# Performance work log

Hardware: AMD Instinct MI355X
Metric: run time of the kernel (lower is better)

Reference implementation:

```python
import jax, jax.numpy as jnp
import numpy as np

B, T, I, H, C = 64, 2048, 256, 256, 10


def setup_inputs() -> dict:
    key = jax.random.key(0)
    ks = jax.random.split(key, 8)
    s_i = 1.0 / np.sqrt(H)
    return {
        "x": jax.random.normal(ks[0], (B, T, I), dtype=jnp.float32),
        "key_mat": jax.random.normal(ks[1], (I, I), dtype=jnp.float32) * (1.0 / np.sqrt(I)),
        "W_ih": jax.random.uniform(ks[2], (4 * H, I), jnp.float32, -s_i, s_i),
        "W_hh": jax.random.uniform(ks[3], (4 * H, H), jnp.float32, -s_i, s_i),
        "b_ih": jax.random.uniform(ks[4], (4 * H,), jnp.float32, -s_i, s_i),
        "b_hh": jax.random.uniform(ks[5], (4 * H,), jnp.float32, -s_i, s_i),
        "W_cls": jax.random.uniform(ks[6], (C, H), jnp.float32, -s_i, s_i),
        "b_cls": jax.random.uniform(ks[7], (C,), jnp.float32, -s_i, s_i),
    }


def reference(x, key_mat, W_ih, W_hh, b_ih, b_hh, W_cls, b_cls):
    # Keyed LSTM: each timestep input is multiplied by the key matrix before
    # the standard LSTM gate computation. Applying the key per step is
    # mathematically identical to one batched matmul up front.
    xk = jnp.einsum("bti,ij->btj", x, key_mat)              # [B,T,I]
    # Precompute input projections for all timesteps (gate order: i,f,g,o)
    x_proj = jnp.einsum("btj,gj->btg", xk, W_ih) + b_ih      # [B,T,4H]

    def step(carry, xt):
        h, c = carry
        gates = xt + h @ W_hh.T + b_hh                        # [B,4H]
        i_g, f_g, g_g, o_g = jnp.split(gates, 4, axis=-1)
        i_g = jax.nn.sigmoid(i_g)
        f_g = jax.nn.sigmoid(f_g)
        g_g = jnp.tanh(g_g)
        o_g = jax.nn.sigmoid(o_g)
        c = f_g * c + i_g * g_g
        h = o_g * jnp.tanh(c)
        return (h, c), None

    h0 = jnp.zeros((x.shape[0], W_hh.shape[1]), x.dtype)
    (h_last, _), _ = jax.lax.scan(step, (h0, h0), jnp.swapaxes(x_proj, 0, 1))
    return h_last @ W_cls.T + b_cls                           # [B,C]
```

## Files before the change

kernel.cpp:

```cpp
#include <hip/hip_runtime.h>
#include <hip/hip_bf16.h>
#include <stdint.h>

#define BB   64
#define TT   2048
#define II   256
#define HH   256
#define G4   1024
#define NC   10

typedef _Float16 half2v __attribute__((ext_vector_type(2)));
typedef _Float16 half8v __attribute__((ext_vector_type(8)));
typedef float    float4v __attribute__((ext_vector_type(4)));

__device__ __forceinline__ float sigmf(float v) { return 1.f / (1.f + __expf(-v)); }
__device__ __forceinline__ float tanhf2(float v) { float e = __expf(2.f * v); return 1.f - 2.f / (e + 1.f); }

__device__ __forceinline__ void bar_lds() {
  asm volatile("s_waitcnt lgkmcnt(0)\n\ts_barrier" ::: "memory");
}

__global__ __launch_bounds__(1024) void prep_wc(
    const float* __restrict__ key, const float* __restrict__ Wih,
    const float* __restrict__ bih, const float* __restrict__ bhh,
    _Float16* __restrict__ WcT, float* __restrict__ biasc) {
  __shared__ float krow[II];
  const int i = blockIdx.x;
  const int g = threadIdx.x;
  if (g < II) krow[g] = key[(size_t)i * II + g];
  __syncthreads();
  const float4* w4 = (const float4*)(Wih + (size_t)g * II);
  float acc = 0.f;
#pragma unroll 8
  for (int j = 0; j < II / 4; ++j) {
    float4 w = w4[j];
    acc += w.x * krow[4 * j] + w.y * krow[4 * j + 1] + w.z * krow[4 * j + 2] + w.w * krow[4 * j + 3];
  }
  WcT[(size_t)g * II + i] = (_Float16)acc;
  if (i == 0) biasc[g] = bih[g] + bhh[g];
}

__global__ __launch_bounds__(256) void prep_wfrag(
    const float* __restrict__ Whh, uint4* __restrict__ wreg, uint4* __restrict__ wldsG) {
  const int id = blockIdx.x * 256 + threadIdx.x;
  const int lane = id & 63;
  const int m  = (id >> 6) & 7;
  const int w  = (id >> 9) & 7;
  const int kt = (id >> 12) & 7;
  const int row = w * 128 + m * 16 + (lane & 15);
  const int k0  = kt * 32 + (lane >> 4) * 8;
  half8v frag;
#pragma unroll
  for (int jj = 0; jj < 8; ++jj) frag[jj] = (_Float16)Whh[(size_t)row * HH + k0 + jj];
  uint4 u = __builtin_bit_cast(uint4, frag);
  if (kt < 6) wreg[((kt * 8 + w) * 8 + m) * 64 + lane] = u;
  else        wldsG[(((kt - 6) * 8 + w) * 8 + m) * 64 + lane] = u;
}

__global__ __launch_bounds__(256) void gemm_xproj(
    const float* __restrict__ x, const _Float16* __restrict__ WcT,
    const float* __restrict__ biasc, _Float16* __restrict__ xpk) {
  __shared__ __align__(16) _Float16 Asm[128][40];
  __shared__ __align__(16) _Float16 Bsm[128][40];
  const int t = threadIdx.x;
  const int n0 = blockIdx.x * 128;
  const int m0 = blockIdx.y * 128;
  const int r = t >> 1;
  const int hoff = (t & 1) * 16;
  const int lane = t & 63, wave = t >> 6;
  const int quad = lane >> 4, l15 = lane & 15;
  const int mh = (wave & 1) * 64, nh = (wave >> 1) * 64;
  float4v zero = {0.f, 0.f, 0.f, 0.f};
  float4v acc[4][4];
#pragma unroll
  for (int a = 0; a < 4; ++a)
#pragma unroll
    for (int b = 0; b < 4; ++b) acc[a][b] = zero;

  for (int kt = 0; kt < 8; ++kt) {
    const int k0 = kt * 32;
    const float4* xa = (const float4*)(x + (size_t)(m0 + r) * II + k0 + hoff);
    float4 f0 = xa[0], f1 = xa[1], f2 = xa[2], f3 = xa[3];
    half8v lo = {(_Float16)f0.x, (_Float16)f0.y, (_Float16)f0.z, (_Float16)f0.w,
                 (_Float16)f1.x, (_Float16)f1.y, (_Float16)f1.z, (_Float16)f1.w};
    half8v hi = {(_Float16)f2.x, (_Float16)f2.y, (_Float16)f2.z, (_Float16)f2.w,
                 (_Float16)f3.x, (_Float16)f3.y, (_Float16)f3.z, (_Float16)f3.w};
    const half8v* bsrc = (const half8v*)(WcT + (size_t)(n0 + r) * II + k0 + hoff);
    half8v b0 = bsrc[0], b1 = bsrc[1];
    *(half8v*)&Asm[r][hoff]     = lo;
    *(half8v*)&Asm[r][hoff + 8] = hi;
    *(half8v*)&Bsm[r][hoff]     = b0;
    *(half8v*)&Bsm[r][hoff + 8] = b1;
    __syncthreads();
    half8v af[4], bf[4];
#pragma unroll
    for (int mt = 0; mt < 4; ++mt) af[mt] = *(const half8v*)&Asm[mh + mt * 16 + l15][quad * 8];
#pragma unroll
    for (int nt = 0; nt < 4; ++nt) bf[nt] = *(const half8v*)&Bsm[nh + nt * 16 + l15][quad * 8];
#pragma unroll
    for (int mt = 0; mt < 4; ++mt)
#pragma unroll
      for (int nt = 0; nt < 4; ++nt)
        acc[mt][nt] = __builtin_amdgcn_mfma_f32_16x16x32_f16(af[mt], bf[nt], acc[mt][nt], 0, 0, 0);
    __syncthreads();
  }
  _Float16* dst = xpk;
#pragma unroll
  for (int nt = 0; nt < 4; ++nt) {
    const int col = n0 + nh + nt * 16 + l15;
    const float bias = biasc[col];
    const int slot16 = (col & 255) * 4 + (col >> 8);
#pragma unroll
    for (int mt = 0; mt < 4; ++mt) {
      const int mrow = m0 + mh + mt * 16 + quad * 4;
#pragma unroll
      for (int j = 0; j < 4; ++j)
        dst[(size_t)(mrow + j) * 1024 + slot16] = (_Float16)(acc[mt][nt][j] + bias);
    }
  }
}

__global__ __launch_bounds__(512, 2) void lstm_seq(
    const uint32_t* __restrict__ xpk, const uint4* __restrict__ wreg,
    const uint4* __restrict__ wldsG, float* __restrict__ hfin) {
  __shared__ __align__(16) _Float16 wsmh[2 * 8 * 8 * 64 * 8];
  __shared__ __align__(16) _Float16 hsh[256];
  __shared__ __align__(16) float gsh[G4];
  const int t0 = threadIdx.x, b = blockIdx.x;
  const int w = t0 >> 6, lane = t0 & 63, quad = lane >> 4;

  half8v wA[48];
#pragma unroll
  for (int kt = 0; kt < 6; ++kt)
#pragma unroll
    for (int m = 0; m < 8; ++m)
      wA[kt * 8 + m] = __builtin_bit_cast(half8v, wreg[((kt * 8 + w) * 8 + m) * 64 + lane]);
#pragma unroll
  for (int i = 0; i < 16; ++i)
    ((uint4*)wsmh)[i * 512 + t0] = wldsG[i * 512 + t0];
  if (t0 < 128) ((uint32_t*)hsh)[t0] = 0;

  float cst = 0.f, hlast = 0.f;
  const uint2* xq = (const uint2*)xpk + (size_t)b * TT * 256 + t0;
  uint2 xn = {0u, 0u};
  if (t0 < 256) xn = xq[0];
  __syncthreads();

  const float4v zero = {0.f, 0.f, 0.f, 0.f};
  for (int t = 0; t < TT; ++t) {
    const uint2 xw = xn;
    if (t0 < 256) xn = xq[(size_t)((t + 1) & (TT - 1)) * 256];
    float4v acc[8];
#pragma unroll
    for (int kt = 0; kt < 8; ++kt) {
      half8v bf = *(const half8v*)&hsh[kt * 32 + quad * 8];
      if (kt < 6) {
#pragma unroll
        for (int m = 0; m < 8; ++m)
          acc[m] = __builtin_amdgcn_mfma_f32_16x16x32_f16(
              wA[kt * 8 + m], bf, (kt == 0) ? zero : acc[m], 0, 0, 0);
      } else {
#pragma unroll
        for (int m = 0; m < 8; ++m) {
          half8v wf = *(const half8v*)&wsmh[((((kt - 6) * 8 + w) * 8 + m) * 64 + lane) * 8];
          acc[m] = __builtin_amdgcn_mfma_f32_16x16x32_f16(wf, bf, acc[m], 0, 0, 0);
        }
      }
    }
    if ((lane & 15) == 0) {
#pragma unroll
      for (int m = 0; m < 8; ++m)
        *(float4v*)&gsh[w * 128 + m * 16 + quad * 4] = acc[m];
    }
    bar_lds();
    if (t0 < 256) {
      float gi = gsh[t0], gf = gsh[t0 + 256], gg = gsh[t0 + 512], go = gsh[t0 + 768];
      half2v xa = __builtin_bit_cast(half2v, xw.x);
      half2v xb = __builtin_bit_cast(half2v, xw.y);
      float ig = sigmf(gi + (float)xa.x);
      float fg = sigmf(gf + (float)xa.y);
      float g2 = tanhf2(gg + (float)xb.x);
      float og = sigmf(go + (float)xb.y);
      cst = fg * cst + ig * g2;
      hlast = og * tanhf2(cst);
      hsh[t0] = (_Float16)hlast;
    }
    bar_lds();
  }
  if (t0 < 256) hfin[(size_t)b * HH + t0] = hlast;
}

__global__ __launch_bounds__(256) void cls_k(
    const float* __restrict__ hfin, const float* __restrict__ Wcls,
    const float* __restrict__ bcls, float* __restrict__ out) {
  __shared__ float part[4][NC];
  const int b = blockIdx.x, tid = threadIdx.x;
  const int lane = tid & 63, wave = tid >> 6;
  float hv = hfin[(size_t)b * HH + tid];
#pragma unroll
  for (int c = 0; c < NC; ++c) {
    float p = hv * Wcls[c * HH + tid];
#pragma unroll
    for (int off = 32; off >= 1; off >>= 1) p += __shfl_down(p, off, 64);
    if (lane == 0) part[wave][c] = p;
  }
  __syncthreads();
  if (tid < NC) {
    out[(size_t)b * NC + tid] =
        part[0][tid] + part[1][tid] + part[2][tid] + part[3][tid] + bcls[tid];
  }
}

extern "C" void kernel_launch(void* const* d_in, const int* in_sizes, int n_in,
                              void* d_out, int out_size, void* d_ws, size_t ws_size,
                              hipStream_t stream) {
  (void)in_sizes; (void)n_in; (void)out_size; (void)ws_size;
  const float* x    = (const float*)d_in[0];
  const float* key  = (const float*)d_in[1];
  const float* Wih  = (const float*)d_in[2];
  const float* Whh  = (const float*)d_in[3];
  const float* bih  = (const float*)d_in[4];
  const float* bhh  = (const float*)d_in[5];
  const float* Wcls = (const float*)d_in[6];
  const float* bcls = (const float*)d_in[7];
  float* out = (float*)d_out;

  char* ws = (char*)d_ws;
  size_t off = 0;
  uint32_t* xpk  = (uint32_t*)(ws + off); off += (size_t)BB * TT * 512 * 4;
  uint4* wreg    = (uint4*)(ws + off);    off += (size_t)6 * 8 * 8 * 64 * 16;
  uint4* wldsG   = (uint4*)(ws + off);    off += (size_t)2 * 8 * 8 * 64 * 16;
  _Float16* WcT  = (_Float16*)(ws + off); off += (size_t)G4 * II * 2;
  float* biasc   = (float*)(ws + off);    off += (size_t)G4 * 4;
  float* hfin    = (float*)(ws + off);    off += (size_t)BB * HH * 4;

  hipLaunchKernelGGL(prep_wc,   dim3(II),  dim3(G4),  0, stream, key, Wih, bih, bhh, WcT, biasc);
  hipLaunchKernelGGL(prep_wfrag, dim3(128), dim3(256), 0, stream, Whh, wreg, wldsG);
  hipLaunchKernelGGL(gemm_xproj, dim3(G4 / 128, (BB * TT) / 128), dim3(256), 0, stream,
                     x, WcT, biasc, (_Float16*)xpk);
  hipLaunchKernelGGL(lstm_seq, dim3(BB), dim3(512), 0, stream,
                     xpk, wreg, wldsG, hfin);
  hipLaunchKernelGGL(cls_k,    dim3(BB), dim3(256), 0, stream, hfin, Wcls, bcls, out);
}
```

Measured before the change: 4.535 ms.

## Batch 16 sequences per LSTM block using full MFMA N dimension with gate-interleaved rows

The recurrent kernel now processes 16 batch elements per workgroup, using the 16 columns of each MFMA tile for batch instead of a single broadcast hidden vector. W_hh rows are permuted so the four gates of one hidden unit land in one accumulator, which lets the epilogue run directly from registers without the gate shared-memory round trip. The hidden-state fragment layout in LDS changes to match. This cuts the grid from 64 to 4 blocks, so per-step latency grows with 16x the useful MFMA work but far fewer CUs are used, and x-projection loads become strided per lane.

New measurement: 13.76 ms. +203.5%, slower.

```diff
diff --git a/kernel.cpp b/kernel.cpp
--- a/kernel.cpp
+++ b/kernel.cpp
@@ -41,20 +41,26 @@
 }
 
 __global__ __launch_bounds__(256) void prep_wfrag(
-    const float* __restrict__ Whh, uint4* __restrict__ wreg, uint4* __restrict__ wldsG) {
+    const float* __restrict__ Whh, uint4* __restrict__ wrg, uint4* __restrict__ wld) {
   const int id = blockIdx.x * 256 + threadIdx.x;
   const int lane = id & 63;
-  const int m  = (id >> 6) & 7;
-  const int w  = (id >> 9) & 7;
-  const int kt = (id >> 12) & 7;
-  const int row = w * 128 + m * 16 + (lane & 15);
-  const int k0  = kt * 32 + (lane >> 4) * 8;
+  const int mg  = (id >> 6) & 63;
+  const int kt  = id >> 12;
+  const int w = mg >> 3, m = mg & 7;
+  const int rowp = mg * 16 + (lane & 15);
+  const int g = (rowp & 3) * 256 + (rowp >> 2);
+  const int k0 = kt * 32 + (lane >> 4) * 8;
   half8v frag;
 #pragma unroll
-  for (int jj = 0; jj < 8; ++jj) frag[jj] = (_Float16)Whh[(size_t)row * HH + k0 + jj];
+  for (int jj = 0; jj < 8; ++jj) frag[jj] = (_Float16)Whh[(size_t)g * HH + k0 + jj];
   uint4 u = __builtin_bit_cast(uint4, frag);
-  if (kt < 6) wreg[((kt * 8 + w) * 8 + m) * 64 + lane] = u;
-  else        wldsG[(((kt - 6) * 8 + w) * 8 + m) * 64 + lane] = u;
+  const bool tail = (kt >= 6) || (kt == 5 && m >= 6);
+  if (!tail) {
+    wrg[((kt * 8 + m) * 8 + w) * 64 + lane] = u;
+  } else {
+    const int slot = (kt == 5) ? (m - 6) : (2 + (kt - 6) * 8 + m);
+    wld[(slot * 8 + w) * 64 + lane] = u;
+  }
 }
 
 __global__ __launch_bounds__(256) void gemm_xproj(
@@ -121,73 +127,74 @@
 }
 
 __global__ __launch_bounds__(512, 2) void lstm_seq(
-    const uint32_t* __restrict__ xpk, const uint4* __restrict__ wreg,
-    const uint4* __restrict__ wldsG, float* __restrict__ hfin) {
-  __shared__ __align__(16) _Float16 wsmh[2 * 8 * 8 * 64 * 8];
-  __shared__ __align__(16) _Float16 hsh[256];
-  __shared__ __align__(16) float gsh[G4];
-  const int t0 = threadIdx.x, b = blockIdx.x;
-  const int w = t0 >> 6, lane = t0 & 63, quad = lane >> 4;
-
-  half8v wA[48];
+    const uint2* __restrict__ xpk, const uint4* __restrict__ wrg,
+    const uint4* __restrict__ wld, float* __restrict__ hfin) {
+  __shared__ __align__(16) uint4 wsm[18 * 512];
+  __shared__ __align__(16) _Float16 hfr[4096];
+  const int t0 = threadIdx.x;
+  const int w = t0 >> 6, lane = t0 & 63;
+  const int l15 = lane & 15, quad = lane >> 4;
+  const int bb = blockIdx.x * 16;
+
+  half8v wA[46];
 #pragma unroll
   for (int kt = 0; kt < 6; ++kt)
 #pragma unroll
-    for (int m = 0; m < 8; ++m)
-      wA[kt * 8 + m] = __builtin_bit_cast(half8v, wreg[((kt * 8 + w) * 8 + m) * 64 + lane]);
-#pragma unroll
-  for (int i = 0; i < 16; ++i)
-    ((uint4*)wsmh)[i * 512 + t0] = wldsG[i * 512 + t0];
-  if (t0 < 128) ((uint32_t*)hsh)[t0] = 0;
-
-  float cst = 0.f, hlast = 0.f;
-  const uint2* xq = (const uint2*)xpk + (size_t)b * TT * 256 + t0;
-  uint2 xn = {0u, 0u};
-  if (t0 < 256) xn = xq[0];
+    for (int m = 0; m < 8; ++m) {
+      if (kt == 5 && m >= 6) continue;
+      wA[kt * 8 + m] = __builtin_bit_cast(half8v, wrg[((kt * 8 + m) * 8 + w) * 64 + lane]);
+    }
+#pragma unroll
+  for (int i = 0; i < 18; ++i) wsm[i * 512 + t0] = wld[i * 512 + t0];
+#pragma unroll
+  for (int i = 0; i < 4; ++i) ((uint32_t*)hfr)[i * 512 + t0] = 0;
+
+  float c0 = 0.f, c1 = 0.f, c2 = 0.f, c3 = 0.f, c4 = 0.f, c5 = 0.f, c6 = 0.f, c7 = 0.f;
+  const size_t xbase = ((size_t)(bb + l15) * TT) * 256 + (size_t)(w * 32 + quad);
   __syncthreads();
 
   const float4v zero = {0.f, 0.f, 0.f, 0.f};
   for (int t = 0; t < TT; ++t) {
-    const uint2 xw = xn;
-    if (t0 < 256) xn = xq[(size_t)((t + 1) & (TT - 1)) * 256];
+    const size_t xo = xbase + (size_t)t * 256;
+    uint2 x0 = xpk[xo], x1 = xpk[xo + 4], x2 = xpk[xo + 8], x3 = xpk[xo + 12];
+    uint2 x4, x5, x6, x7;
     float4v acc[8];
 #pragma unroll
     for (int kt = 0; kt < 8; ++kt) {
-      half8v bf = *(const half8v*)&hsh[kt * 32 + quad * 8];
-      if (kt < 6) {
-#pragma unroll
-        for (int m = 0; m < 8; ++m)
-          acc[m] = __builtin_amdgcn_mfma_f32_16x16x32_f16(
-              wA[kt * 8 + m], bf, (kt == 0) ? zero : acc[m], 0, 0, 0);
-      } else {
-#pragma unroll
-        for (int m = 0; m < 8; ++m) {
-          half8v wf = *(const half8v*)&wsmh[((((kt - 6) * 8 + w) * 8 + m) * 64 + lane) * 8];
-          acc[m] = __builtin_amdgcn_mfma_f32_16x16x32_f16(wf, bf, acc[m], 0, 0, 0);
+      half8v hb = *(const half8v*)&hfr[kt * 512 + lane * 8];
+      if (kt == 6) { x4 = xpk[xo + 16]; x5 = xpk[xo + 20]; x6 = xpk[xo + 24]; x7 = xpk[xo + 28]; }
+#pragma unroll
+      for (int m = 0; m < 8; ++m) {
+        half8v wf;
+        if (kt < 5 || (kt == 5 && m < 6)) {
+          wf = wA[kt * 8 + m];
+        } else {
+          const int slot = (kt == 5) ? (m - 6) : (2 + (kt - 6) * 8 + m);
+          wf = __builtin_bit_cast(half8v, wsm[slot * 512 + t0]);
         }
+        acc[m] = __builtin_amdgcn_mfma_f32_16x16x32_f16(wf, hb, (kt == 0) ? zero : acc[m], 0, 0, 0);
       }
     }
-    if ((lane & 15) == 0) {
-#pragma unroll
-      for (int m = 0; m < 8; ++m)
-        *(float4v*)&gsh[w * 128 + m * 16 + quad * 4] = acc[m];
-    }
     bar_lds();
-    if (t0 < 256) {
-      float gi = gsh[t0], gf = gsh[t0 + 256], gg = gsh[t0 + 512], go = gsh[t0 + 768];
-      half2v xa = __builtin_bit_cast(half2v, xw.x);
-      half2v xb = __builtin_bit_cast(half2v, xw.y);
-      float ig = sigmf(gi + (float)xa.x);
-      float fg = sigmf(gf + (float)xa.y);
-      float g2 = tanhf2(gg + (float)xb.x);
-      float og = sigmf(go + (float)xb.y);
-      cst = fg * cst + ig * g2;
-      hlast = og * tanhf2(cst);
-      hsh[t0] = (_Float16)hlast;
-    }
+#define EPI(m, xv, cs)                                                        \
+    {                                                                         \
+      half2v xa = __builtin_bit_cast(half2v, (xv).x);           \
+      half2v xb = __builtin_bit_cast(half2v, (xv).y);           \
+      float ig = sigmf(acc[m][0] + (float)xa.x);                              \
+      float fg = sigmf(acc[m][1] + (float)xa.y);                              \
+      float gg = tanhf2(acc[m][2] + (float)xb.x);                             \
+      float og = sigmf(acc[m][3] + (float)xb.y);                              \
+      cs = fg * cs + ig * gg;                                                 \
+      float hh = og * tanhf2(cs);                                             \
+      const int ke = (m) * 4 + quad;                                          \
+      hfr[w * 512 + ((ke >> 3) * 16 + l15) * 8 + (ke & 7)] = (_Float16)hh;    \
+      if (t == TT - 1) hfin[(size_t)(bb + l15) * HH + (w * 32 + ke)] = hh;    \
+    }
+    EPI(0, x0, c0) EPI(1, x1, c1) EPI(2, x2, c2) EPI(3, x3, c3)
+    EPI(4, x4, c4) EPI(5, x5, c5) EPI(6, x6, c6) EPI(7, x7, c7)
+#undef EPI
     bar_lds();
   }
-  if (t0 < 256) hfin[(size_t)b * HH + t0] = hlast;
 }
 
 __global__ __launch_bounds__(256) void cls_k(
@@ -227,18 +234,18 @@
 
   char* ws = (char*)d_ws;
   size_t off = 0;
-  uint32_t* xpk  = (uint32_t*)(ws + off); off += (size_t)BB * TT * 512 * 4;
-  uint4* wreg    = (uint4*)(ws + off);    off += (size_t)6 * 8 * 8 * 64 * 16;
-  uint4* wldsG   = (uint4*)(ws + off);    off += (size_t)2 * 8 * 8 * 64 * 16;
+  uint2* xpk     = (uint2*)(ws + off);    off += (size_t)BB * TT * 512 * 4;
+  uint4* wrg     = (uint4*)(ws + off);    off += (size_t)48 * 8 * 64 * 16;
+  uint4* wld     = (uint4*)(ws + off);    off += (size_t)18 * 8 * 64 * 16;
   _Float16* WcT  = (_Float16*)(ws + off); off += (size_t)G4 * II * 2;
   float* biasc   = (float*)(ws + off);    off += (size_t)G4 * 4;
   float* hfin    = (float*)(ws + off);    off += (size_t)BB * HH * 4;
 
-  hipLaunchKernelGGL(prep_wc,   dim3(II),  dim3(G4),  0, stream, key, Wih, bih, bhh, WcT, biasc);
-  hipLaunchKernelGGL(prep_wfrag, dim3(128), dim3(256), 0, stream, Whh, wreg, wldsG);
+  hipLaunchKernelGGL(prep_wc,    dim3(II),  dim3(G4),  0, stream, key, Wih, bih, bhh, WcT, biasc);
+  hipLaunchKernelGGL(prep_wfrag, dim3(128), dim3(256), 0, stream, Whh, wrg, wld);
   hipLaunchKernelGGL(gemm_xproj, dim3(G4 / 128, (BB * TT) / 128), dim3(256), 0, stream,
                      x, WcT, biasc, (_Float16*)xpk);
-  hipLaunchKernelGGL(lstm_seq, dim3(BB), dim3(512), 0, stream,
-                     xpk, wreg, wldsG, hfin);
+  hipLaunchKernelGGL(lstm_seq, dim3(BB / 16), dim3(512), 0, stream,
+                     xpk, wrg, wld, hfin);
   hipLaunchKernelGGL(cls_k,    dim3(BB), dim3(256), 0, stream, hfin, Wcls, bcls, out);
 }
```
